# Optimization experiments

Hardware: AMD Instinct MI355X
Metric: run time of the kernel (lower is better)

## Reference

```python
import jax, jax.numpy as jnp
import numpy as np

B, T, C, H = 2, 2048, 1024, 16
D = C // H  # head dim, even
NEG = -1e10  # masked_fill value used by the torch module (not -inf)


def _rope_cache(dim, max_positions):
    # Faithful to source: theta_i = 1/10000**(-2*(i-1)/dim), i = arange(dim//2)
    i = jnp.arange(dim // 2, dtype=jnp.float32)
    theta = 1.0 / (10000.0 ** (-2.0 * (i - 1.0) / dim))
    ang = jnp.arange(max_positions, dtype=jnp.float32)[:, None] * theta[None, :]  # [T, D/2]
    return jnp.cos(ang), jnp.sin(ang)


def _apply_rope(x, cos, sin):
    # x: [B,H,T,D]; consecutive pairs form complex numbers (x[...,2j], x[...,2j+1])
    xp = x.reshape(*x.shape[:-1], D // 2, 2)
    xr, xi = xp[..., 0], xp[..., 1]
    rr = xr * cos - xi * sin
    ri = xr * sin + xi * cos
    return jnp.stack([rr, ri], axis=-1).reshape(x.shape)


def setup_inputs() -> dict:
    key = jax.random.key(0)
    ks = jax.random.split(key, 5)
    s = 1.0 / np.sqrt(C)
    return {
        'x': jax.random.normal(ks[0], (B, T, C), jnp.float32),
        'Wq': jax.random.normal(ks[1], (C, C), jnp.float32) * s,
        'bq': jnp.zeros((C,), jnp.float32),
        'Wk': jax.random.normal(ks[2], (C, C), jnp.float32) * s,
        'bk': jnp.zeros((C,), jnp.float32),
        'Wv': jax.random.normal(ks[3], (C, C), jnp.float32) * s,
        'bv': jnp.zeros((C,), jnp.float32),
        'Wp': jax.random.normal(ks[4], (C, C), jnp.float32) * s,
        'bp': jnp.zeros((C,), jnp.float32),
    }


def reference(x, Wq, bq, Wk, bk, Wv, bv, Wp, bp):
    cos, sin = _rope_cache(D, T)  # [T, D/2]
    def split_heads(h):
        return h.reshape(B, T, H, D).transpose(0, 2, 1, 3)  # [B,H,T,D]
    q = split_heads(x @ Wq.T + bq)
    k = split_heads(x @ Wk.T + bk)
    v = split_heads(x @ Wv.T + bv)
    q = _apply_rope(q, cos, sin)
    k = _apply_rope(k, cos, sin)
    att = jnp.einsum('bhqd,bhkd->bhqk', q, k) * (1.0 / np.sqrt(D))  # [B,H,T,T]
    causal = jnp.tril(jnp.ones((T, T), bool))
    att = jnp.where(causal, att, NEG)
    att = jax.nn.softmax(att, axis=-1)
    y = jnp.einsum('bhqk,bhkd->bhqd', att, v)
    y = y.transpose(0, 2, 1, 3).reshape(B, T, C)
    return y @ Wp.T + bp
```

## Files before the change

kernel.cpp:

```cpp
#include <hip/hip_runtime.h>

#define SEQ 2048
#define CDIM 1024
#define NHEAD 16
#define HDIM 64
#define NSLOT 80

typedef __bf16 bf16x8 __attribute__((ext_vector_type(8)));
typedef __bf16 bf16x4v __attribute__((ext_vector_type(4)));
typedef float f32x4 __attribute__((ext_vector_type(4)));

typedef const __attribute__((address_space(1))) char* gcp_t;
typedef __attribute__((address_space(3))) char* lcp_t;

__device__ __forceinline__ void gload16(const void* g, void* l) {
    __builtin_amdgcn_global_load_lds((gcp_t)g, (lcp_t)l, 16, 0, 0);
}

__device__ __forceinline__ unsigned short f2bf(float f) {
    unsigned int u = __float_as_uint(f);
    u += 0x7fffu + ((u >> 16) & 1u);
    return (unsigned short)(u >> 16);
}

__device__ __forceinline__ float bflo(unsigned int u) { return __uint_as_float(u << 16); }
__device__ __forceinline__ float bfhi(unsigned int u) { return __uint_as_float(u & 0xffff0000u); }


__global__ void cvt_kernel(const float* __restrict__ src, unsigned short* __restrict__ dst, int n4) {
    int i = blockIdx.x * blockDim.x + threadIdx.x;
    if (i < n4) {
        float4 v = ((const float4*)src)[i];
        ushort4 o;
        o.x = f2bf(v.x); o.y = f2bf(v.y); o.z = f2bf(v.z); o.w = f2bf(v.w);
        ((ushort4*)dst)[i] = o;
    }
}

__global__ void cvtw_kernel(const float* __restrict__ Wq, const float* __restrict__ Wk,
                            const float* __restrict__ Wv, const float* __restrict__ Wp,
                            unsigned short* __restrict__ wqkv, unsigned short* __restrict__ wpb) {
    int i = blockIdx.x * blockDim.x + threadIdx.x;
    int which = i >> 18, r = i & 262143;
    const float* s = (which == 0) ? Wq : (which == 1) ? Wk : (which == 2) ? Wv : Wp;
    unsigned short* d = (which < 3) ? (wqkv + (size_t)which * 1048576) : wpb;
    float4 v = ((const float4*)s)[r];
    ushort4 o;
    o.x = f2bf(v.x); o.y = f2bf(v.y); o.z = f2bf(v.z); o.w = f2bf(v.w);
    ((ushort4*)d)[r] = o;
}

__global__ void rope_kernel(float2* __restrict__ cstab) {
    int idx = blockIdx.x * blockDim.x + threadIdx.x;
    int j = idx & 31, t = idx >> 5;
    float e = -2.0f * ((float)j - 1.0f) / 64.0f;
    float denom = (float)pow(10000.0, (double)e);
    float theta = 1.0f / denom;
    float ang = (float)t * theta;
    cstab[idx] = make_float2(cosf(ang), sinf(ang));
}

template <int MODE>
__global__ __launch_bounds__(256) void gemm_bt(
    const unsigned short* __restrict__ A, const unsigned short* __restrict__ Bm,
    const float* __restrict__ b0, const float* __restrict__ b1, const float* __restrict__ b2,
    unsigned short* __restrict__ qb, unsigned short* __restrict__ kb,
    unsigned short* __restrict__ vtb, float* __restrict__ outf,
    const float2* __restrict__ cstab)
{
    constexpr int K = 1024;
    constexpr int NIT = K / 32;
    __shared__ __align__(16) unsigned short As[2][128 * 32];
    __shared__ __align__(16) unsigned short Bs[2][128 * 32];
    const int tid = threadIdx.x, lane = tid & 63, wid = tid >> 6;
    const int m0 = blockIdx.y * 128, n0 = blockIdx.x * 128;
    const int wr = wid >> 1, wc = wid & 1;

    f32x4 acc[4][4] = {};

    const char* Ag = (const char*)(A + (size_t)m0 * K);
    const char* Bg = (const char*)(Bm + (size_t)n0 * K);
    const int r0 = tid >> 2, cb = (tid & 3) * 16;
    const int r1 = r0 + 64;
    const int ldsw = wid << 10;

    auto stage = [&](int k0, int bufi) {
        gload16(Ag + (size_t)r0 * 2048 + k0 * 2 + cb, (char*)As[bufi] + ldsw);
        gload16(Ag + (size_t)r1 * 2048 + k0 * 2 + cb, (char*)As[bufi] + 4096 + ldsw);
        gload16(Bg + (size_t)r0 * 2048 + k0 * 2 + cb, (char*)Bs[bufi] + ldsw);
        gload16(Bg + (size_t)r1 * 2048 + k0 * 2 + cb, (char*)Bs[bufi] + 4096 + ldsw);
    };

    stage(0, 0);
    __syncthreads();

    for (int it = 0; it < NIT; ++it) {
        const int cur = it & 1;
        if (it + 1 < NIT) stage((it + 1) * 32, cur ^ 1);
        bf16x8 af[4], bfr[4];
#pragma unroll
        for (int am = 0; am < 4; ++am)
            af[am] = *(const bf16x8*)(As[cur] + (wr * 64 + am * 16 + (lane & 15)) * 32 + (lane >> 4) * 8);
#pragma unroll
        for (int an = 0; an < 4; ++an)
            bfr[an] = *(const bf16x8*)(Bs[cur] + (wc * 64 + an * 16 + (lane & 15)) * 32 + (lane >> 4) * 8);
#pragma unroll
        for (int am = 0; am < 4; ++am)
#pragma unroll
            for (int an = 0; an < 4; ++an)
                acc[am][an] = __builtin_amdgcn_mfma_f32_16x16x32_bf16(af[am], bfr[an], acc[am][an], 0, 0, 0);
        __syncthreads();
    }

    if (MODE == 0) {
        const float QSCL = 0.18033688011112042f;
#pragma unroll
        for (int an = 0; an < 4; ++an) {
            const int ng = n0 + wc * 64 + an * 16 + (lane & 15);
            const int which = ng >> 10, nl = ng & 1023;
            const int h = nl >> 6, d = nl & 63;
            const float* bptr = (which == 0) ? b0 : (which == 1) ? b1 : b2;
            const float bias = bptr[nl];
            if (which < 2) {
                unsigned short* dst = (which == 0) ? qb : kb;
                const float qs = (which == 0) ? QSCL : 1.0f;
                const int j = d >> 1;
#pragma unroll
                for (int am = 0; am < 4; ++am) {
#pragma unroll
                    for (int i = 0; i < 4; ++i) {
                        const int row = m0 + wr * 64 + am * 16 + (lane >> 4) * 4 + i;
                        const int bb = row >> 11, t = row & 2047;
                        float v = acc[am][an][i] + bias;
                        float p = __shfl_xor(v, 1);
                        const float2 cs = cstab[t * 32 + j];
                        v = (d & 1) ? fmaf(v, cs.x, p * cs.y) : fmaf(v, cs.x, -p * cs.y);
                        dst[((size_t)((bb * 16 + h) * 2048 + t)) * 64 + d] = f2bf(v * qs);
                    }
                }
            } else {
#pragma unroll
                for (int am = 0; am < 4; ++am) {
                    const int rowb = m0 + wr * 64 + am * 16 + (lane >> 4) * 4;
                    const int bb = rowb >> 11, t = rowb & 2047;
                    ushort4 pk;
                    pk.x = f2bf(acc[am][an][0] + bias);
                    pk.y = f2bf(acc[am][an][1] + bias);
                    pk.z = f2bf(acc[am][an][2] + bias);
                    pk.w = f2bf(acc[am][an][3] + bias);
                    *(ushort4*)(vtb + ((size_t)((bb * 16 + h) * 64 + d)) * 2048 + t) = pk;
                }
            }
        }
    } else {
#pragma unroll
        for (int an = 0; an < 4; ++an) {
            const int col = n0 + wc * 64 + an * 16 + (lane & 15);
            const float bias = b0[col];
#pragma unroll
            for (int am = 0; am < 4; ++am)
#pragma unroll
                for (int i = 0; i < 4; ++i) {
                    const int row = m0 + wr * 64 + am * 16 + (lane >> 4) * 4 + i;
                    outf[(size_t)row * 1024 + col] = acc[am][an][i] + bias;
                }
        }
    }
}

__global__ __launch_bounds__(256) void attn_kernel(
    const unsigned short* __restrict__ qb, const unsigned short* __restrict__ kb,
    const unsigned short* __restrict__ vtb, unsigned short* __restrict__ pb,
    float2* __restrict__ ml)
{
    __shared__ __align__(16) unsigned short Ks[2][64 * 64];
    __shared__ __align__(16) unsigned short Vs[2][64 * 64];
    __shared__ __align__(16) unsigned short Ps[4][16 * 64];
    const int tid = threadIdx.x, lane = tid & 63, wid = tid >> 6;
    const int bh = blockIdx.x;
    const int y = blockIdx.y;
    int qt, ck, nc;
    if (y < 32)      { qt = 31 - (y >> 2); ck = y & 3; nc = 4; }
    else if (y < 56) { int t2 = y - 32; int k3 = t2 / 3; qt = 23 - k3; ck = t2 - k3 * 3; nc = 3; }
    else if (y < 72) { int t2 = y - 56; qt = 15 - (t2 >> 1); ck = t2 & 1; nc = 2; }
    else             { qt = 7 - (y - 72); ck = 0; nc = 1; }
    const int nt = qt + 1;
    const int t0 = ck * nt / nc, t1 = (ck + 1) * nt / nc;
    const int q0 = qt * 64;
    const int qw = q0 + wid * 16;
    const unsigned short* Qg = qb + (size_t)bh * SEQ * HDIM;
    const char* Kg = (const char*)(kb + (size_t)bh * SEQ * HDIM);
    const char* Vg = (const char*)(vtb + (size_t)bh * HDIM * SEQ);

    bf16x8 qf[2];
#pragma unroll
    for (int kf = 0; kf < 2; ++kf)
        qf[kf] = *(const bf16x8*)(Qg + (size_t)(qw + (lane & 15)) * 64 + kf * 32 + (lane >> 4) * 8);

    f32x4 o[4] = {};
    float mrun = -3e38f;
    float lrun = 0.0f;

    const int cr0 = tid >> 3, cc0 = ((tid & 7) * 16) ^ ((cr0 & 7) << 4);
    const int cr1 = cr0 + 32, cc1 = ((tid & 7) * 16) ^ ((cr1 & 7) << 4);
    const int ldsw = wid << 10;

    auto stage = [&](int kt, int bufi) {
        const size_t kv0 = (size_t)kt * 64;
        gload16(Kg + (kv0 + cr0) * 128 + cc0, (char*)Ks[bufi] + ldsw);
        gload16(Kg + (kv0 + cr1) * 128 + cc1, (char*)Ks[bufi] + 4096 + ldsw);
        gload16(Vg + (size_t)cr0 * 4096 + kv0 * 2 + cc0, (char*)Vs[bufi] + ldsw);
        gload16(Vg + (size_t)cr1 * 4096 + kv0 * 2 + cc1, (char*)Vs[bufi] + 4096 + ldsw);
    };

    stage(t0, 0);
    __syncthreads();

    for (int kt = t0; kt < t1; ++kt) {
        const int cur = (kt - t0) & 1;
        if (kt + 1 < t1) stage(kt + 1, cur ^ 1);
        const int kv0 = kt * 64;
        {
            f32x4 s[4] = {};
            __builtin_amdgcn_s_setprio(1);
#pragma unroll
            for (int kf = 0; kf < 2; ++kf) {
                bf16x8 kfr[4];
#pragma unroll
                for (int an = 0; an < 4; ++an) {
                    const int r = an * 16 + (lane & 15);
                    kfr[an] = *(const bf16x8*)((const char*)Ks[cur] + r * 128 + ((kf * 64 + (lane >> 4) * 16) ^ ((r & 7) << 4)));
                }
#pragma unroll
                for (int an = 0; an < 4; ++an)
                    s[an] = __builtin_amdgcn_mfma_f32_16x16x32_bf16(kfr[an], qf[kf], s[an], 0, 0, 0);
            }
            __builtin_amdgcn_s_setprio(0);
            const bool need_mask = (kv0 + 63 > qw);
            const int qg = qw + (lane & 15);
            const int kbase = kv0 + ((lane >> 4) << 2);
            float p[4][4];
            float mx = -3e38f;
#pragma unroll
            for (int an = 0; an < 4; ++an)
#pragma unroll
                for (int i = 0; i < 4; ++i) {
                    float v = s[an][i];
                    if (need_mask && (kbase + an * 16 + i > qg)) v = -3e38f;
                    p[an][i] = v;
                    mx = fmaxf(mx, v);
                }
            mx = fmaxf(mx, __shfl_xor(mx, 16));
            mx = fmaxf(mx, __shfl_xor(mx, 32));
            if (!__all(mx <= mrun + 8.0f)) {
                const float mnew = fmaxf(mrun, mx);
                const float fsc = __builtin_amdgcn_exp2f(mrun - mnew);
                lrun *= fsc;
#pragma unroll
                for (int dn = 0; dn < 4; ++dn) o[dn] *= fsc;
                mrun = mnew;
            }
            float rs = 0.0f;
#pragma unroll
            for (int an = 0; an < 4; ++an)
#pragma unroll
                for (int i = 0; i < 4; ++i) {
                    p[an][i] = __builtin_amdgcn_exp2f(p[an][i] - mrun);
                    rs += p[an][i];
                }
            rs += __shfl_xor(rs, 16);
            rs += __shfl_xor(rs, 32);
            lrun += rs;
            const int ql = lane & 15;
            char* pbs = (char*)Ps[wid] + ql * 128;
            const int xr = (ql & 7) << 4;
            const int gb = (lane >> 4) << 3;
#pragma unroll
            for (int an = 0; an < 4; ++an) {
                bf16x4v pk;
                pk[0] = (__bf16)p[an][0]; pk[1] = (__bf16)p[an][1];
                pk[2] = (__bf16)p[an][2]; pk[3] = (__bf16)p[an][3];
                *(bf16x4v*)(pbs + ((an * 32 + gb) ^ xr)) = pk;
            }
            __builtin_amdgcn_s_setprio(1);
#pragma unroll
            for (int kf = 0; kf < 2; ++kf) {
                bf16x8 vf[4], pf;
#pragma unroll
                for (int dn = 0; dn < 4; ++dn) {
                    const int r = dn * 16 + (lane & 15);
                    vf[dn] = *(const bf16x8*)((const char*)Vs[cur] + r * 128 + ((kf * 64 + (lane >> 4) * 16) ^ ((r & 7) << 4)));
                }
                {
                    const int qlr = lane & 15;
                    pf = *(const bf16x8*)((const char*)Ps[wid] + qlr * 128 + ((kf * 64 + (lane >> 4) * 16) ^ ((qlr & 7) << 4)));
                }
#pragma unroll
                for (int dn = 0; dn < 4; ++dn)
                    o[dn] = __builtin_amdgcn_mfma_f32_16x16x32_bf16(vf[dn], pf, o[dn], 0, 0, 0);
            }
            __builtin_amdgcn_s_setprio(0);
        }
        __syncthreads();
    }

    {
        const size_t sbase = (size_t)bh * NSLOT + y;
        const int qloc = wid * 16 + (lane & 15);
        unsigned short* prow = pb + (sbase * 64 + qloc) * 64;
#pragma unroll
        for (int dn = 0; dn < 4; ++dn) {
            const int d = dn * 16 + ((lane >> 4) << 2);
            bf16x4v pk;
            pk[0] = (__bf16)o[dn][0];
            pk[1] = (__bf16)o[dn][1];
            pk[2] = (__bf16)o[dn][2];
            pk[3] = (__bf16)o[dn][3];
            *(bf16x4v*)(prow + d) = pk;
        }
        if ((lane >> 4) == 0) ml[sbase * 64 + qloc] = make_float2(mrun, lrun);
    }
}

__global__ __launch_bounds__(256) void combine_kernel(
    const unsigned short* __restrict__ pb, const float2* __restrict__ ml,
    unsigned short* __restrict__ yb)
{
    const int qt = blockIdx.x, bh = blockIdx.y;
    const int b = bh >> 4, h = bh & 15;
    int base, nc;
    if (qt >= 24)      { base = (31 - qt) * 4;      nc = 4; }
    else if (qt >= 16) { base = 32 + (23 - qt) * 3; nc = 3; }
    else if (qt >= 8)  { base = 56 + (15 - qt) * 2; nc = 2; }
    else               { base = 72 + (7 - qt);      nc = 1; }
    const int t = threadIdx.x;
    const int q = t >> 2;
    const int d0 = (t & 3) * 16;
    const size_t sbase = (size_t)bh * NSLOT + base;

    float m[4], l[4];
    float M = -3e38f;
#pragma unroll
    for (int c = 0; c < 4; ++c)
        if (c < nc) {
            float2 v = ml[(sbase + c) * 64 + q];
            m[c] = v.x; l[c] = v.y;
            M = fmaxf(M, v.x);
        }
    float L = 0.0f;
    float w[4];
#pragma unroll
    for (int c = 0; c < 4; ++c)
        if (c < nc) {
            w[c] = __builtin_amdgcn_exp2f(m[c] - M);
            L += l[c] * w[c];
        }
    const float invL = 1.0f / L;

    float acc[16] = {};
#pragma unroll
    for (int c = 0; c < 4; ++c)
        if (c < nc) {
            const float wc = w[c] * invL;
            const uint4* src = (const uint4*)(pb + ((sbase + c) * 64 + q) * 64 + d0);
            uint4 A = src[0], B = src[1];
            const unsigned int ua[8] = {A.x, A.y, A.z, A.w, B.x, B.y, B.z, B.w};
#pragma unroll
            for (int k = 0; k < 8; ++k) {
                acc[2 * k]     = fmaf(wc, bflo(ua[k]), acc[2 * k]);
                acc[2 * k + 1] = fmaf(wc, bfhi(ua[k]), acc[2 * k + 1]);
            }
        }

    unsigned int outw[8];
#pragma unroll
    for (int k = 0; k < 8; ++k)
        outw[k] = (unsigned int)f2bf(acc[2 * k]) | ((unsigned int)f2bf(acc[2 * k + 1]) << 16);
    uint4* dst = (uint4*)(yb + (size_t)(b * SEQ + qt * 64 + q) * CDIM + h * 64 + d0);
    dst[0] = make_uint4(outw[0], outw[1], outw[2], outw[3]);
    dst[1] = make_uint4(outw[4], outw[5], outw[6], outw[7]);
}


extern "C" void kernel_launch(void* const* d_in, const int* in_sizes, int n_in,
                              void* d_out, int out_size, void* d_ws, size_t ws_size,
                              hipStream_t stream) {
    (void)in_sizes; (void)n_in; (void)out_size; (void)ws_size;
    const float* x  = (const float*)d_in[0];
    const float* Wq = (const float*)d_in[1];
    const float* bq = (const float*)d_in[2];
    const float* Wk = (const float*)d_in[3];
    const float* bk = (const float*)d_in[4];
    const float* Wv = (const float*)d_in[5];
    const float* bv = (const float*)d_in[6];
    const float* Wp = (const float*)d_in[7];
    const float* bp = (const float*)d_in[8];
    float* out = (float*)d_out;

    char* ws = (char*)d_ws;
    size_t off = 0;
    auto take = [&](size_t bytes) -> char* {
        char* p = ws + off;
        off = (off + bytes + 255) & ~(size_t)255;
        return p;
    };
    float2* cstab = (float2*)take((size_t)SEQ * 32 * 8);
    unsigned short* xb   = (unsigned short*)take((size_t)4096 * 1024 * 2);
    unsigned short* wqkv = (unsigned short*)take((size_t)3 * 1024 * 1024 * 2);
    unsigned short* wpb  = (unsigned short*)take((size_t)1024 * 1024 * 2);
    unsigned short* qbuf = (unsigned short*)take((size_t)32 * SEQ * HDIM * 2);
    unsigned short* kbuf = (unsigned short*)take((size_t)32 * SEQ * HDIM * 2);
    unsigned short* vtb  = (unsigned short*)take((size_t)32 * HDIM * SEQ * 2);
    unsigned short* yb   = (unsigned short*)take((size_t)4096 * 1024 * 2);
    unsigned short* pbuf = (unsigned short*)take((size_t)32 * NSLOT * 64 * 64 * 2);
    float2* mlb          = (float2*)take((size_t)32 * NSLOT * 64 * 8);

    rope_kernel<<<256, 256, 0, stream>>>(cstab);
    cvt_kernel<<<4096, 256, 0, stream>>>(x, xb, 1048576);
    cvtw_kernel<<<4096, 256, 0, stream>>>(Wq, Wk, Wv, Wp, wqkv, wpb);

    dim3 g0(24, 32);
    gemm_bt<0><<<g0, 256, 0, stream>>>(xb, wqkv, bq, bk, bv, qbuf, kbuf, vtb, nullptr, cstab);
    dim3 g1(32, NSLOT);
    attn_kernel<<<g1, 256, 0, stream>>>(qbuf, kbuf, vtb, pbuf, mlb);
    dim3 gc(32, 32);
    combine_kernel<<<gc, 256, 0, stream>>>(pbuf, mlb, yb);
    dim3 g2(8, 32);
    gemm_bt<1><<<g2, 256, 0, stream>>>(yb, wpb, bp, nullptr, nullptr, nullptr, nullptr, nullptr, out, cstab);
}
```

Before: 140.5 us.

## Triple-buffer GEMM LDS with swizzle, grid remap, and smaller output-projection tiles

```diff
diff --git a/kernel.cpp b/kernel.cpp
--- a/kernel.cpp
+++ b/kernel.cpp
@@ -25,6 +25,8 @@
 
 __device__ __forceinline__ float bflo(unsigned int u) { return __uint_as_float(u << 16); }
 __device__ __forceinline__ float bfhi(unsigned int u) { return __uint_as_float(u & 0xffff0000u); }
+
+__device__ __forceinline__ int swz16(int r) { return ((r >> 1) & 3) << 4; }
 
 
 __global__ void cvt_kernel(const float* __restrict__ src, unsigned short* __restrict__ dst, int n4) {
@@ -60,7 +62,7 @@
     cstab[idx] = make_float2(cosf(ang), sinf(ang));
 }
 
-template <int MODE>
+template <int MODE, int BM, int NXT, int NYT>
 __global__ __launch_bounds__(256) void gemm_bt(
     const unsigned short* __restrict__ A, const unsigned short* __restrict__ Bm,
     const float* __restrict__ b0, const float* __restrict__ b1, const float* __restrict__ b2,
@@ -70,53 +72,81 @@
 {
     constexpr int K = 1024;
     constexpr int NIT = K / 32;
-    __shared__ __align__(16) unsigned short As[2][128 * 32];
-    __shared__ __align__(16) unsigned short Bs[2][128 * 32];
+    constexpr int NR = (BM == 128) ? 4 : 2;
+    constexpr int ABYTES = BM * 64;
+    constexpr int BBYTES = 128 * 64;
+    __shared__ __align__(16) char As[3][ABYTES];
+    __shared__ __align__(16) char Bs[3][BBYTES];
     const int tid = threadIdx.x, lane = tid & 63, wid = tid >> 6;
-    const int m0 = blockIdx.y * 128, n0 = blockIdx.x * 128;
-    const int wr = wid >> 1, wc = wid & 1;
-
-    f32x4 acc[4][4] = {};
+    constexpr int NWG = NXT * NYT;
+    const int bid = blockIdx.x;
+    const int swz = (bid & 7) * (NWG >> 3) + (bid >> 3);
+    const int mt = swz / NXT;
+    const int m0 = mt * BM, n0 = (swz - mt * NXT) * 128;
+    const int wr = (BM == 128) ? ((wid >> 1) * 64) : 0;
+    const int wc = (BM == 128) ? ((wid & 1) * 64) : (wid * 32);
+
+    f32x4 acc[4][NR] = {};
 
     const char* Ag = (const char*)(A + (size_t)m0 * K);
     const char* Bg = (const char*)(Bm + (size_t)n0 * K);
     const int r0 = tid >> 2, cb = (tid & 3) * 16;
-    const int r1 = r0 + 64;
     const int ldsw = wid << 10;
 
     auto stage = [&](int k0, int bufi) {
-        gload16(Ag + (size_t)r0 * 2048 + k0 * 2 + cb, (char*)As[bufi] + ldsw);
-        gload16(Ag + (size_t)r1 * 2048 + k0 * 2 + cb, (char*)As[bufi] + 4096 + ldsw);
-        gload16(Bg + (size_t)r0 * 2048 + k0 * 2 + cb, (char*)Bs[bufi] + ldsw);
-        gload16(Bg + (size_t)r1 * 2048 + k0 * 2 + cb, (char*)Bs[bufi] + 4096 + ldsw);
+        char* Ad = As[bufi];
+        char* Bd = Bs[bufi];
+        gload16(Ag + (size_t)r0 * 2048 + k0 * 2 + (cb ^ swz16(r0)), Ad + ldsw);
+        if (BM == 128)
+            gload16(Ag + (size_t)(r0 + 64) * 2048 + k0 * 2 + (cb ^ swz16(r0 + 64)), Ad + 4096 + ldsw);
+        gload16(Bg + (size_t)r0 * 2048 + k0 * 2 + (cb ^ swz16(r0)), Bd + ldsw);
+        gload16(Bg + (size_t)(r0 + 64) * 2048 + k0 * 2 + (cb ^ swz16(r0 + 64)), Bd + 4096 + ldsw);
     };
 
     stage(0, 0);
-    __syncthreads();
-
+    stage(32, 1);
+
+    int cur = 0;
     for (int it = 0; it < NIT; ++it) {
-        const int cur = it & 1;
-        if (it + 1 < NIT) stage((it + 1) * 32, cur ^ 1);
-        bf16x8 af[4], bfr[4];
+        if (it + 1 < NIT) {
+            if constexpr (BM == 128) asm volatile("s_waitcnt vmcnt(4)" ::: "memory");
+            else                     asm volatile("s_waitcnt vmcnt(3)" ::: "memory");
+        } else {
+            asm volatile("s_waitcnt vmcnt(0)" ::: "memory");
+        }
+        __builtin_amdgcn_s_barrier();
+        asm volatile("" ::: "memory");
+        if (it + 2 < NIT) {
+            int nxt2 = cur + 2; if (nxt2 >= 3) nxt2 -= 3;
+            stage((it + 2) * 32, nxt2);
+        }
+        const char* Ac = As[cur];
+        const char* Bc = Bs[cur];
+        const int fs = (lane >> 4) * 16;
+        bf16x8 af[4], bfr[NR];
+#pragma unroll
+        for (int am = 0; am < 4; ++am) {
+            const int r = wr + am * 16 + (lane & 15);
+            af[am] = *(const bf16x8*)(Ac + r * 64 + (fs ^ swz16(r)));
+        }
+#pragma unroll
+        for (int an = 0; an < NR; ++an) {
+            const int r = wc + an * 16 + (lane & 15);
+            bfr[an] = *(const bf16x8*)(Bc + r * 64 + (fs ^ swz16(r)));
+        }
 #pragma unroll
         for (int am = 0; am < 4; ++am)
-            af[am] = *(const bf16x8*)(As[cur] + (wr * 64 + am * 16 + (lane & 15)) * 32 + (lane >> 4) * 8);
-#pragma unroll
-        for (int an = 0; an < 4; ++an)
-            bfr[an] = *(const bf16x8*)(Bs[cur] + (wc * 64 + an * 16 + (lane & 15)) * 32 + (lane >> 4) * 8);
-#pragma unroll
-        for (int am = 0; am < 4; ++am)
-#pragma unroll
-            for (int an = 0; an < 4; ++an)
+#pragma unroll
+            for (int an = 0; an < NR; ++an)
                 acc[am][an] = __builtin_amdgcn_mfma_f32_16x16x32_bf16(af[am], bfr[an], acc[am][an], 0, 0, 0);
-        __syncthreads();
+        cur = (cur == 2) ? 0 : cur + 1;
     }
 
     if (MODE == 0) {
         const float QSCL = 0.18033688011112042f;
 #pragma unroll
-        for (int an = 0; an < 4; ++an) {
-            const int ng = n0 + wc * 64 + an * 16 + (lane & 15);
+        for (int an = 0; an < NR; ++an) {
+            const int ng = n0 + wc + an * 16 + (lane & 15);
             const int which = ng >> 10, nl = ng & 1023;
             const int h = nl >> 6, d = nl & 63;
             const float* bptr = (which == 0) ? b0 : (which == 1) ? b1 : b2;
@@ -129,7 +159,7 @@
                 for (int am = 0; am < 4; ++am) {
 #pragma unroll
                     for (int i = 0; i < 4; ++i) {
-                        const int row = m0 + wr * 64 + am * 16 + (lane >> 4) * 4 + i;
+                        const int row = m0 + wr + am * 16 + (lane >> 4) * 4 + i;
                         const int bb = row >> 11, t = row & 2047;
                         float v = acc[am][an][i] + bias;
                         float p = __shfl_xor(v, 1);
@@ -141,7 +171,7 @@
             } else {
 #pragma unroll
                 for (int am = 0; am < 4; ++am) {
-                    const int rowb = m0 + wr * 64 + am * 16 + (lane >> 4) * 4;
+                    const int rowb = m0 + wr + am * 16 + (lane >> 4) * 4;
                     const int bb = rowb >> 11, t = rowb & 2047;
                     ushort4 pk;
                     pk.x = f2bf(acc[am][an][0] + bias);
@@ -154,14 +184,14 @@
         }
     } else {
 #pragma unroll
-        for (int an = 0; an < 4; ++an) {
-            const int col = n0 + wc * 64 + an * 16 + (lane & 15);
+        for (int an = 0; an < NR; ++an) {
+            const int col = n0 + wc + an * 16 + (lane & 15);
             const float bias = b0[col];
 #pragma unroll
             for (int am = 0; am < 4; ++am)
 #pragma unroll
                 for (int i = 0; i < 4; ++i) {
-                    const int row = m0 + wr * 64 + am * 16 + (lane >> 4) * 4 + i;
+                    const int row = m0 + wr + am * 16 + (lane >> 4) * 4 + i;
                     outf[(size_t)row * 1024 + col] = acc[am][an][i] + bias;
                 }
         }
@@ -419,12 +449,10 @@
     cvt_kernel<<<4096, 256, 0, stream>>>(x, xb, 1048576);
     cvtw_kernel<<<4096, 256, 0, stream>>>(Wq, Wk, Wv, Wp, wqkv, wpb);
 
-    dim3 g0(24, 32);
-    gemm_bt<0><<<g0, 256, 0, stream>>>(xb, wqkv, bq, bk, bv, qbuf, kbuf, vtb, nullptr, cstab);
+    gemm_bt<0, 128, 24, 32><<<768, 256, 0, stream>>>(xb, wqkv, bq, bk, bv, qbuf, kbuf, vtb, nullptr, cstab);
     dim3 g1(32, NSLOT);
     attn_kernel<<<g1, 256, 0, stream>>>(qbuf, kbuf, vtb, pbuf, mlb);
     dim3 gc(32, 32);
     combine_kernel<<<gc, 256, 0, stream>>>(pbuf, mlb, yb);
-    dim3 g2(8, 32);
-    gemm_bt<1><<<g2, 256, 0, stream>>>(yb, wpb, bp, nullptr, nullptr, nullptr, nullptr, nullptr, out, cstab);
-}
+    gemm_bt<1, 64, 8, 64><<<512, 256, 0, stream>>>(yb, wpb, bp, nullptr, nullptr, nullptr, nullptr, nullptr, out, cstab);
+}
```

After: 146.8 us. 4.5% more time.
